# Performance work log

Measured on AMD Instinct MI355X. Metric: run time of the kernel, lower is better.

Reference implementation:

```python
import jax, jax.numpy as jnp
import numpy as np

B, H, S, D = 2, 16, 2048, 64


def _apply_rope(feats, cos, sin):
    # feats: [B,H,S,D]; cos,sin: [B,S,D//2] -> broadcast over heads
    c = cos[:, None, :, :]
    s = sin[:, None, :, :]
    x1, x2 = jnp.split(feats, 2, axis=-1)
    r1 = x1 * c - x2 * s
    r2 = x1 * s + x2 * c
    return jnp.concatenate([r1, r2], axis=-1)


def setup_inputs() -> dict:
    key = jax.random.key(0)
    kq, kk, kv, ka = jax.random.split(key, 4)
    q = jax.random.normal(kq, (B, H, S, D), dtype=jnp.float32)
    k = jax.random.normal(kk, (B, H, S, D), dtype=jnp.float32)
    v = jax.random.normal(kv, (B, H, S, D), dtype=jnp.float32)
    # geometry-derived rope angles -> cos/sin coefficients
    angles = jax.random.uniform(ka, (B, S, D // 2), dtype=jnp.float32,
                                minval=-np.pi, maxval=np.pi)
    return {"q": q, "k": k, "v": v,
            "cos": jnp.cos(angles), "sin": jnp.sin(angles)}


def reference(q, k, v, cos, sin):
    # Ray-conditioned RoPE on Q and K, then scaled dot-product attention.
    qr = _apply_rope(q, cos, sin)
    kr = _apply_rope(k, cos, sin)
    scale = 1.0 / jnp.sqrt(jnp.asarray(q.shape[-1], q.dtype))
    scores = jnp.einsum('bhqd,bhkd->bhqk', qr, kr) * scale  # [B,H,S,S]
    attn = jax.nn.softmax(scores, axis=-1)
    return jnp.einsum('bhqk,bhkd->bhqd', attn, v)
```

## Files before the change

kernel.cpp:

```cpp
#include <hip/hip_runtime.h>

#define NB 2
#define NH 16
#define SEQ 2048
#define DIM 64
#define SD (SEQ * DIM)

typedef short s16x8 __attribute__((ext_vector_type(8)));
typedef float f32x4 __attribute__((ext_vector_type(4)));
typedef float f32x16 __attribute__((ext_vector_type(16)));
typedef unsigned u32x4 __attribute__((ext_vector_type(4)));

typedef const __attribute__((address_space(1))) void* gas_t;
typedef __attribute__((address_space(3))) void* las_t;

__device__ __forceinline__ short f2bf(float f) {
  unsigned u = __float_as_uint(f);
  u += 0x7FFFu + ((u >> 16) & 1u);
  return (short)(u >> 16);
}

__device__ __forceinline__ float fast_exp2(float x) {
#if __has_builtin(__builtin_amdgcn_exp2f)
  return __builtin_amdgcn_exp2f(x);
#else
  float r;
  asm("v_exp_f32 %0, %1" : "=v"(r) : "v"(x));
  return r;
#endif
}

__global__ __launch_bounds__(256)
void prep_all(const float* __restrict__ q, const float* __restrict__ k,
              const float* __restrict__ v, const float* __restrict__ cg,
              const float* __restrict__ sg, short* __restrict__ qr,
              short* __restrict__ kr, short* __restrict__ vt) {
  const int tid = threadIdx.x;
  if (blockIdx.x < 1024) {
    const float QS = 0.125f * 1.44269504088896340736f;
    const int gt = blockIdx.x * 256 + tid;
    const int row = gt >> 2;
    const int dd = (gt & 3) * 8;
    const int s = row & (SEQ - 1);
    const int b = row >> 15;

    const float* qp = q + (size_t)row * DIM;
    const float* kp = k + (size_t)row * DIM;
    const float* cp = cg + ((size_t)b * SEQ + s) * (DIM / 2) + dd;
    const float* sp = sg + ((size_t)b * SEQ + s) * (DIM / 2) + dd;

    float q1[8], q2[8], k1[8], k2[8], cc[8], ss[8];
    *(f32x4*)&q1[0] = *(const f32x4*)(qp + dd);
    *(f32x4*)&q1[4] = *(const f32x4*)(qp + dd + 4);
    *(f32x4*)&q2[0] = *(const f32x4*)(qp + dd + 32);
    *(f32x4*)&q2[4] = *(const f32x4*)(qp + dd + 36);
    *(f32x4*)&k1[0] = *(const f32x4*)(kp + dd);
    *(f32x4*)&k1[4] = *(const f32x4*)(kp + dd + 4);
    *(f32x4*)&k2[0] = *(const f32x4*)(kp + dd + 32);
    *(f32x4*)&k2[4] = *(const f32x4*)(kp + dd + 36);
    *(f32x4*)&cc[0] = *(const f32x4*)(cp);
    *(f32x4*)&cc[4] = *(const f32x4*)(cp + 4);
    *(f32x4*)&ss[0] = *(const f32x4*)(sp);
    *(f32x4*)&ss[4] = *(const f32x4*)(sp + 4);

    s16x8 qo1, qo2, ko1, ko2;
#pragma unroll
    for (int j = 0; j < 8; ++j) {
      qo1[j] = f2bf((q1[j] * cc[j] - q2[j] * ss[j]) * QS);
      qo2[j] = f2bf((q1[j] * ss[j] + q2[j] * cc[j]) * QS);
      ko1[j] = f2bf(k1[j] * cc[j] - k2[j] * ss[j]);
      ko2[j] = f2bf(k1[j] * ss[j] + k2[j] * cc[j]);
    }
    *(s16x8*)&qr[(size_t)row * DIM + dd] = qo1;
    *(s16x8*)&qr[(size_t)row * DIM + dd + 32] = qo2;
    *(s16x8*)&kr[(size_t)row * DIM + dd] = ko1;
    *(s16x8*)&kr[(size_t)row * DIM + dd + 32] = ko2;
  } else {
    const int blk = blockIdx.x - 1024;
    const int bh = blk >> 5;
    const int tile = blk & 31;
    const int d = tid & 63;
    const int kg = tid >> 6;
    const float* vp = v + ((size_t)bh * SEQ + tile * 64 + kg * 16) * DIM + d;
    short* op = vt + (size_t)bh * SD + (size_t)(tile * 2 + (kg >> 1)) * (64 * 32)
                + d * 32 + (kg & 1) * 16;
    s16x8 w0, w1;
#pragma unroll
    for (int j = 0; j < 8; ++j) w0[j] = f2bf(vp[(size_t)j * DIM]);
#pragma unroll
    for (int j = 0; j < 8; ++j) w1[j] = f2bf(vp[(size_t)(j + 8) * DIM]);
    *(s16x8*)&op[0] = w0;
    *(s16x8*)&op[8] = w1;
  }
}

__global__ __launch_bounds__(256, 4)
void attn_main(const short* __restrict__ qr, const short* __restrict__ kr,
               const short* __restrict__ vt, float* __restrict__ out) {
  __shared__ __align__(16) short Kb[2][2][32 * 64];
  __shared__ __align__(16) short Vb[2][2][64 * 32];
  __shared__ float lred[2][32];

  const int nq = SEQ / 64;
  const int bid = blockIdx.x;
  const int cpx = gridDim.x >> 3;
  const int swz = (bid & 7) * cpx + (bid >> 3);
  const int bh = swz / nq;
  const int qb = swz % nq;

  const int tid = threadIdx.x;
  const int w = tid >> 6;
  const int kh = w >> 1;
  const int qs = w & 1;
  const int lane = tid & 63;
  const int n = lane & 31;
  const int h = lane >> 5;

  const int qw = qb * 64 + qs * 32;

  const short* qrp = qr + (size_t)bh * SD + (size_t)(qw + n) * DIM + 8 * h;
  s16x8 qa[4];
#pragma unroll
  for (int ds = 0; ds < 4; ++ds) qa[ds] = *(const s16x8*)(qrp + 16 * ds);

  int koff[2], voff[2];
#pragma unroll
  for (int i = 0; i < 2; ++i) {
    const int p = qs * 128 + i * 64 + lane;
    const int krow = p >> 3, kslot = p & 7;
    koff[i] = krow * 128 + ((kslot ^ (krow & 7)) * 16);
    const int vrow = p >> 2, vslot = p & 3;
    voff[i] = vrow * 64 + ((vslot ^ ((vrow >> 1) & 3)) * 16);
  }
  const char* kbh = (const char*)(kr + (size_t)bh * SD);
  const char* vbh = (const char*)(vt + (size_t)bh * SD);
  const int tbase = kh * 32;

  f32x16 Oa[2];
  Oa[0] = {};
  Oa[1] = {};
  float lp = 0.f;

#define STAGE(buf, t)                                                               \
  do {                                                                              \
    const char* ks_ = kbh + (size_t)(t) * 4096;                                     \
    const char* vs_ = vbh + (size_t)(t) * 4096;                                     \
    __builtin_amdgcn_global_load_lds((gas_t)(ks_ + koff[0]),                        \
                                     (las_t)&Kb[kh][buf][qs * 1024], 16, 0, 0);     \
    __builtin_amdgcn_global_load_lds((gas_t)(ks_ + koff[1]),                        \
                                     (las_t)&Kb[kh][buf][qs * 1024 + 512], 16, 0, 0); \
    __builtin_amdgcn_global_load_lds((gas_t)(vs_ + voff[0]),                        \
                                     (las_t)&Vb[kh][buf][qs * 1024], 16, 0, 0);     \
    __builtin_amdgcn_global_load_lds((gas_t)(vs_ + voff[1]),                        \
                                     (las_t)&Vb[kh][buf][qs * 1024 + 512], 16, 0, 0); \
  } while (0)

  STAGE(0, tbase);
  __syncthreads();
  int cur = 0;

#pragma unroll 2
  for (int it = 0; it < 32; ++it) {
    if (it < 31) STAGE(cur ^ 1, tbase + it + 1);

    s16x8 kf[4], vf[2][2];
#pragma unroll
    for (int ds = 0; ds < 4; ++ds)
      kf[ds] = *(const s16x8*)&Kb[kh][cur][n * 64 + (((2 * ds + h) ^ (n & 7)) * 8)];
#pragma unroll
    for (int dsub = 0; dsub < 2; ++dsub)
#pragma unroll
      for (int ks = 0; ks < 2; ++ks)
        vf[dsub][ks] = *(const s16x8*)&Vb[kh][cur][(dsub * 32 + n) * 32 +
                                                   (((2 * ks + h) ^ ((n >> 1) & 3)) * 8)];

    f32x16 S = {};
#pragma unroll
    for (int ds = 0; ds < 4; ++ds)
      S = __builtin_amdgcn_mfma_f32_32x32x16_bf16(kf[ds], qa[ds], S, 0, 0, 0);

    float e[16];
#pragma unroll
    for (int r = 0; r < 16; ++r) e[r] = fast_exp2(S[r]);
    {
      float s0 = (e[0] + e[1]) + (e[2] + e[3]);
      float s1 = (e[4] + e[5]) + (e[6] + e[7]);
      float s2 = (e[8] + e[9]) + (e[10] + e[11]);
      float s3 = (e[12] + e[13]) + (e[14] + e[15]);
      lp += (s0 + s1) + (s2 + s3);
    }

    unsigned pk[8];
#pragma unroll
    for (int i = 0; i < 8; ++i)
      asm("v_cvt_pk_bf16_f32 %0, %1, %2" : "=v"(pk[i]) : "v"(e[2 * i]), "v"(e[2 * i + 1]));
    s16x8 pa[2];
#pragma unroll
    for (int ksl = 0; ksl < 2; ++ksl) {
      unsigned a0 = pk[4 * ksl + 0], b0 = pk[4 * ksl + 2];
      unsigned a1 = pk[4 * ksl + 1], b1 = pk[4 * ksl + 3];
      asm("v_permlane32_swap_b32 %0, %1" : "+v"(a0), "+v"(b0));
      asm("v_permlane32_swap_b32 %0, %1" : "+v"(a1), "+v"(b1));
      u32x4 t;
      t[0] = a0; t[1] = a1; t[2] = b0; t[3] = b1;
      pa[ksl] = *(s16x8*)&t;
    }

#pragma unroll
    for (int dsub = 0; dsub < 2; ++dsub)
#pragma unroll
      for (int ksl = 0; ksl < 2; ++ksl)
        Oa[dsub] = __builtin_amdgcn_mfma_f32_32x32x16_bf16(pa[ksl], vf[dsub][ksl],
                                                           Oa[dsub], 0, 0, 0);

    __syncthreads();
    cur ^= 1;
  }
#undef STAGE

  lp += __shfl_xor(lp, 32);

  float* xch = (float*)&Kb[0][0][0];
  if (kh == 1) {
    float* ob = xch + qs * 2048;
#pragma unroll
    for (int r = 0; r < 16; ++r) {
      const int m = (r & 3) + 8 * (r >> 2) + 4 * h;
      ob[m * 64 + n] = Oa[0][r];
      ob[m * 64 + 32 + n] = Oa[1][r];
    }
    if (h == 0) lred[qs][n] = lp;
  }
  __syncthreads();
  if (kh == 0) {
    const float* pb = xch + qs * 2048;
    lp += lred[qs][n];
    const float invq = 1.0f / lp;
    float* og = out + ((size_t)bh * SEQ + qw) * DIM + n;
#pragma unroll
    for (int r = 0; r < 16; ++r) {
      const int m = (r & 3) + 8 * (r >> 2) + 4 * h;
      const float iv = __shfl(invq, m);
      og[(size_t)m * DIM] = (Oa[0][r] + pb[m * 64 + n]) * iv;
      og[(size_t)m * DIM + 32] = (Oa[1][r] + pb[m * 64 + 32 + n]) * iv;
    }
  }
}

__global__ __launch_bounds__(256, 2)
void rope_attn_mono(const float* __restrict__ qg, const float* __restrict__ kgl,
                    const float* __restrict__ vg, const float* __restrict__ cg,
                    const float* __restrict__ sg, float* __restrict__ out) {
  __shared__ __align__(16) short Kt[64 * DIM];
  __shared__ __align__(16) short Vt[DIM * 64];
  __shared__ __align__(16) short Pw[4][16 * 64];
  const int nq = SEQ / 64;
  const int bid = blockIdx.x;
  const int cpx = gridDim.x >> 3;
  const int swz = (bid & 7) * cpx + (bid >> 3);
  const int bh = swz / nq;
  const int qb = swz % nq;
  const int b = bh >> 4;
  const int tid = threadIdx.x;
  const int w = tid >> 6;
  const int lane = tid & 63;
  const int c = lane & 15;
  const int g = lane >> 4;
  const float* qbase = qg + (size_t)bh * SEQ * DIM;
  const float* kbase = kgl + (size_t)bh * SEQ * DIM;
  const float* vbase = vg + (size_t)bh * SEQ * DIM;
  const float* cbase = cg + (size_t)b * SEQ * (DIM / 2);
  const float* sbase = sg + (size_t)b * SEQ * (DIM / 2);
  const float QS = 0.125f * 1.44269504088896340736f;
  const int qrow = qb * 64 + w * 16 + c;
  const int d0 = g * 8;
  s16x8 qa0, qa1;
  {
    const float* qr = qbase + (size_t)qrow * DIM;
    const float* cr = cbase + (size_t)qrow * (DIM / 2);
    const float* sr = sbase + (size_t)qrow * (DIM / 2);
    float x1[8], x2[8], cc[8], ss[8];
    *(f32x4*)&x1[0] = *(const f32x4*)(qr + d0);
    *(f32x4*)&x1[4] = *(const f32x4*)(qr + d0 + 4);
    *(f32x4*)&x2[0] = *(const f32x4*)(qr + d0 + 32);
    *(f32x4*)&x2[4] = *(const f32x4*)(qr + d0 + 36);
    *(f32x4*)&cc[0] = *(const f32x4*)(cr + d0);
    *(f32x4*)&cc[4] = *(const f32x4*)(cr + d0 + 4);
    *(f32x4*)&ss[0] = *(const f32x4*)(sr + d0);
    *(f32x4*)&ss[4] = *(const f32x4*)(sr + d0 + 4);
#pragma unroll
    for (int j = 0; j < 8; ++j) {
      qa0[j] = f2bf((x1[j] * cc[j] - x2[j] * ss[j]) * QS);
      qa1[j] = f2bf((x1[j] * ss[j] + x2[j] * cc[j]) * QS);
    }
  }
  f32x4 Oa[4];
#pragma unroll
  for (int dt = 0; dt < 4; ++dt) { Oa[dt][0] = 0.f; Oa[dt][1] = 0.f; Oa[dt][2] = 0.f; Oa[dt][3] = 0.f; }
  float mrun[4], lrun[4];
#pragma unroll
  for (int r = 0; r < 4; ++r) { mrun[r] = -3.0e38f; lrun[r] = 0.f; }
  for (int kv = 0; kv < SEQ / 64; ++kv) {
    const int s0 = kv * 64;
#pragma unroll
    for (int rep = 0; rep < 2; ++rep) {
      const int id = tid + rep * 256;
      const int key = id >> 3;
      const int u = id & 7;
      const int srow = s0 + key;
      const float* krp = kbase + (size_t)srow * DIM;
      const float* cr = cbase + (size_t)srow * (DIM / 2);
      const float* sr = sbase + (size_t)srow * (DIM / 2);
      const int dd = (u & 3) * 8;
      float a[8], bb[8], cf[8], sf[8];
      *(f32x4*)&a[0] = *(const f32x4*)(krp + dd);
      *(f32x4*)&a[4] = *(const f32x4*)(krp + dd + 4);
      *(f32x4*)&bb[0] = *(const f32x4*)(krp + dd + 32);
      *(f32x4*)&bb[4] = *(const f32x4*)(krp + dd + 36);
      *(f32x4*)&cf[0] = *(const f32x4*)(cr + dd);
      *(f32x4*)&cf[4] = *(const f32x4*)(cr + dd + 4);
      *(f32x4*)&sf[0] = *(const f32x4*)(sr + dd);
      *(f32x4*)&sf[4] = *(const f32x4*)(sr + dd + 4);
      s16x8 wv;
      if (u < 4) {
#pragma unroll
        for (int j = 0; j < 8; ++j) wv[j] = f2bf(a[j] * cf[j] - bb[j] * sf[j]);
      } else {
#pragma unroll
        for (int j = 0; j < 8; ++j) wv[j] = f2bf(a[j] * sf[j] + bb[j] * cf[j]);
      }
      *(s16x8*)&Kt[key * DIM + ((u ^ (key & 7)) * 8)] = wv;
    }
    {
      const int d = tid & 63;
      const int kgp = tid >> 6;
      const float* vrow = vbase + (size_t)(s0 + kgp * 16) * DIM + d;
      s16x8 w0, w1;
#pragma unroll
      for (int j = 0; j < 8; ++j) w0[j] = f2bf(vrow[(size_t)j * DIM]);
#pragma unroll
      for (int j = 0; j < 8; ++j) w1[j] = f2bf(vrow[(size_t)(j + 8) * DIM]);
      *(s16x8*)&Vt[d * 64 + (((2 * kgp) ^ (d & 7)) * 8)] = w0;
      *(s16x8*)&Vt[d * 64 + (((2 * kgp + 1) ^ (d & 7)) * 8)] = w1;
    }
    __syncthreads();
    f32x4 sc[4];
#pragma unroll
    for (int kt = 0; kt < 4; ++kt) {
      const int key = kt * 16 + c;
      s16x8 b0 = *(const s16x8*)&Kt[key * DIM + ((g ^ (key & 7)) * 8)];
      s16x8 b1 = *(const s16x8*)&Kt[key * DIM + (((4 + g) ^ (key & 7)) * 8)];
      f32x4 z = {0.f, 0.f, 0.f, 0.f};
      z = __builtin_amdgcn_mfma_f32_16x16x32_bf16(qa0, b0, z, 0, 0, 0);
      z = __builtin_amdgcn_mfma_f32_16x16x32_bf16(qa1, b1, z, 0, 0, 0);
      sc[kt] = z;
    }
    float pf[4][4];
#pragma unroll
    for (int r = 0; r < 4; ++r) {
      float mt = fmaxf(fmaxf(sc[0][r], sc[1][r]), fmaxf(sc[2][r], sc[3][r]));
#pragma unroll
      for (int msk = 1; msk < 16; msk <<= 1) mt = fmaxf(mt, __shfl_xor(mt, msk));
      const float mnew = fmaxf(mrun[r], mt);
      const float corr = exp2f(mrun[r] - mnew);
      mrun[r] = mnew;
      float rs = 0.f;
#pragma unroll
      for (int kt = 0; kt < 4; ++kt) {
        const float p = exp2f(sc[kt][r] - mnew);
        pf[kt][r] = p;
        rs += p;
      }
#pragma unroll
      for (int msk = 1; msk < 16; msk <<= 1) rs += __shfl_xor(rs, msk);
      lrun[r] = lrun[r] * corr + rs;
#pragma unroll
      for (int dt = 0; dt < 4; ++dt) Oa[dt][r] *= corr;
    }
#pragma unroll
    for (int kt = 0; kt < 4; ++kt) {
      const int u = 2 * kt + (c >> 3);
      const int c7 = c & 7;
#pragma unroll
      for (int r = 0; r < 4; ++r) {
        const int qq = 4 * g + r;
        Pw[w][qq * 64 + ((u ^ (qq & 7)) * 8) + c7] = f2bf(pf[kt][r]);
      }
    }
    {
      const int qq = c;
      s16x8 pa0 = *(const s16x8*)&Pw[w][qq * 64 + ((g ^ (qq & 7)) * 8)];
      s16x8 pa1 = *(const s16x8*)&Pw[w][qq * 64 + (((4 + g) ^ (qq & 7)) * 8)];
#pragma unroll
      for (int dt = 0; dt < 4; ++dt) {
        const int d = dt * 16 + c;
        s16x8 v0 = *(const s16x8*)&Vt[d * 64 + ((g ^ (d & 7)) * 8)];
        s16x8 v1 = *(const s16x8*)&Vt[d * 64 + (((4 + g) ^ (d & 7)) * 8)];
        Oa[dt] = __builtin_amdgcn_mfma_f32_16x16x32_bf16(pa0, v0, Oa[dt], 0, 0, 0);
        Oa[dt] = __builtin_amdgcn_mfma_f32_16x16x32_bf16(pa1, v1, Oa[dt], 0, 0, 0);
      }
    }
    __syncthreads();
  }
  float* ob = out + ((size_t)bh * SEQ + (size_t)qb * 64 + (size_t)(w * 16)) * DIM;
#pragma unroll
  for (int r = 0; r < 4; ++r) {
    const float inv = 1.0f / lrun[r];
#pragma unroll
    for (int dt = 0; dt < 4; ++dt)
      ob[(size_t)(4 * g + r) * DIM + dt * 16 + c] = Oa[dt][r] * inv;
  }
}

extern "C" void kernel_launch(void* const* d_in, const int* in_sizes, int n_in,
                              void* d_out, int out_size, void* d_ws, size_t ws_size,
                              hipStream_t stream) {
  const float* q = (const float*)d_in[0];
  const float* k = (const float*)d_in[1];
  const float* v = (const float*)d_in[2];
  const float* cosv = (const float*)d_in[3];
  const float* sinv = (const float*)d_in[4];
  float* out = (float*)d_out;

  const size_t elems = (size_t)NB * NH * SEQ * DIM;
  const size_t need = 3 * elems * sizeof(short);

  if (ws_size >= need) {
    short* qrw = (short*)d_ws;
    short* krw = qrw + elems;
    short* vtw = krw + elems;
    hipLaunchKernelGGL(prep_all, dim3(2048), dim3(256), 0, stream,
                       q, k, v, cosv, sinv, qrw, krw, vtw);
    hipLaunchKernelGGL(attn_main, dim3(NB * NH * (SEQ / 64)), dim3(256), 0, stream,
                       qrw, krw, vtw, out);
  } else {
    hipLaunchKernelGGL(rope_attn_mono, dim3(NB * NH * (SEQ / 64)), dim3(256), 0, stream,
                       q, k, v, cosv, sinv, out);
  }
}
```

Baseline: 65.13 us.

## Split keys per wave with private LDS staging and no per-iteration barriers

Restructures attn_main so each of the four waves handles all 64 queries of the block over a private quarter of the key sequence. Each wave stages its own K/V tiles into a private double buffer and waits on them with s_waitcnt, which removes the block-wide __syncthreads per iteration and reuses each K/V fragment across two query sub-tiles. A four-way cross-wave reduction of outputs and row sums through LDS, with vectorized float4 stores, replaces the old two-way exchange. In exchange the kernel uses more registers (launch bounds lowered to 2 blocks per SIMD) and more LDS.

```diff
diff --git a/kernel.cpp b/kernel.cpp
--- a/kernel.cpp
+++ b/kernel.cpp
@@ -94,12 +94,11 @@
   }
 }
 
-__global__ __launch_bounds__(256, 4)
+__global__ __launch_bounds__(256, 2)
 void attn_main(const short* __restrict__ qr, const short* __restrict__ kr,
                const short* __restrict__ vt, float* __restrict__ out) {
-  __shared__ __align__(16) short Kb[2][2][32 * 64];
-  __shared__ __align__(16) short Vb[2][2][64 * 32];
-  __shared__ float lred[2][32];
+  __shared__ __align__(16) short St[4][2][4096];
+  __shared__ float lred[4][64];
 
   const int nq = SEQ / 64;
   const int bid = blockIdx.x;
@@ -110,23 +109,23 @@
 
   const int tid = threadIdx.x;
   const int w = tid >> 6;
-  const int kh = w >> 1;
-  const int qs = w & 1;
   const int lane = tid & 63;
   const int n = lane & 31;
   const int h = lane >> 5;
-
-  const int qw = qb * 64 + qs * 32;
-
-  const short* qrp = qr + (size_t)bh * SD + (size_t)(qw + n) * DIM + 8 * h;
-  s16x8 qa[4];
-#pragma unroll
-  for (int ds = 0; ds < 4; ++ds) qa[ds] = *(const s16x8*)(qrp + 16 * ds);
-
-  int koff[2], voff[2];
-#pragma unroll
-  for (int i = 0; i < 2; ++i) {
-    const int p = qs * 128 + i * 64 + lane;
+  const int qw = qb * 64;
+
+  s16x8 qa[2][4];
+#pragma unroll
+  for (int qs = 0; qs < 2; ++qs) {
+    const short* qrp = qr + (size_t)bh * SD + (size_t)(qw + qs * 32 + n) * DIM + 8 * h;
+#pragma unroll
+    for (int ds = 0; ds < 4; ++ds) qa[qs][ds] = *(const s16x8*)(qrp + 16 * ds);
+  }
+
+  int koff[4], voff[4];
+#pragma unroll
+  for (int i = 0; i < 4; ++i) {
+    const int p = i * 64 + lane;
     const int krow = p >> 3, kslot = p & 7;
     koff[i] = krow * 128 + ((kslot ^ (krow & 7)) * 16);
     const int vrow = p >> 2, vslot = p & 3;
@@ -134,115 +133,131 @@
   }
   const char* kbh = (const char*)(kr + (size_t)bh * SD);
   const char* vbh = (const char*)(vt + (size_t)bh * SD);
-  const int tbase = kh * 32;
-
-  f32x16 Oa[2];
-  Oa[0] = {};
-  Oa[1] = {};
-  float lp = 0.f;
-
-#define STAGE(buf, t)                                                               \
-  do {                                                                              \
-    const char* ks_ = kbh + (size_t)(t) * 4096;                                     \
-    const char* vs_ = vbh + (size_t)(t) * 4096;                                     \
-    __builtin_amdgcn_global_load_lds((gas_t)(ks_ + koff[0]),                        \
-                                     (las_t)&Kb[kh][buf][qs * 1024], 16, 0, 0);     \
-    __builtin_amdgcn_global_load_lds((gas_t)(ks_ + koff[1]),                        \
-                                     (las_t)&Kb[kh][buf][qs * 1024 + 512], 16, 0, 0); \
-    __builtin_amdgcn_global_load_lds((gas_t)(vs_ + voff[0]),                        \
-                                     (las_t)&Vb[kh][buf][qs * 1024], 16, 0, 0);     \
-    __builtin_amdgcn_global_load_lds((gas_t)(vs_ + voff[1]),                        \
-                                     (las_t)&Vb[kh][buf][qs * 1024 + 512], 16, 0, 0); \
+  const int tb = w * 16;
+
+  f32x16 Oa[2][2];
+  Oa[0][0] = {}; Oa[0][1] = {}; Oa[1][0] = {}; Oa[1][1] = {};
+  float lp[2] = {0.f, 0.f};
+
+#define STAGE(buf, t)                                                              \
+  do {                                                                             \
+    const char* ks_ = kbh + (size_t)(t) * 4096;                                    \
+    const char* vs_ = vbh + (size_t)(t) * 4096;                                    \
+    __builtin_amdgcn_global_load_lds((gas_t)(ks_ + koff[0]), (las_t)&St[w][buf][0], 16, 0, 0);    \
+    __builtin_amdgcn_global_load_lds((gas_t)(ks_ + koff[1]), (las_t)&St[w][buf][512], 16, 0, 0);  \
+    __builtin_amdgcn_global_load_lds((gas_t)(ks_ + koff[2]), (las_t)&St[w][buf][1024], 16, 0, 0); \
+    __builtin_amdgcn_global_load_lds((gas_t)(ks_ + koff[3]), (las_t)&St[w][buf][1536], 16, 0, 0); \
+    __builtin_amdgcn_global_load_lds((gas_t)(vs_ + voff[0]), (las_t)&St[w][buf][2048], 16, 0, 0); \
+    __builtin_amdgcn_global_load_lds((gas_t)(vs_ + voff[1]), (las_t)&St[w][buf][2560], 16, 0, 0); \
+    __builtin_amdgcn_global_load_lds((gas_t)(vs_ + voff[2]), (las_t)&St[w][buf][3072], 16, 0, 0); \
+    __builtin_amdgcn_global_load_lds((gas_t)(vs_ + voff[3]), (las_t)&St[w][buf][3584], 16, 0, 0); \
   } while (0)
 
-  STAGE(0, tbase);
+  STAGE(0, tb);
+  int cur = 0;
+
+  for (int it = 0; it < 16; ++it) {
+    asm volatile("s_waitcnt lgkmcnt(0)" ::: "memory");
+    if (it < 15) {
+      STAGE(cur ^ 1, tb + it + 1);
+      asm volatile("s_waitcnt vmcnt(8)" ::: "memory");
+    } else {
+      asm volatile("s_waitcnt vmcnt(0)" ::: "memory");
+    }
+    __builtin_amdgcn_sched_barrier(0);
+
+    const short* Kc = &St[w][cur][0];
+    const short* Vc = &St[w][cur][2048];
+    s16x8 kf[4], vf[2][2];
+#pragma unroll
+    for (int ds = 0; ds < 4; ++ds)
+      kf[ds] = *(const s16x8*)&Kc[n * 64 + (((2 * ds + h) ^ (n & 7)) * 8)];
+#pragma unroll
+    for (int dsub = 0; dsub < 2; ++dsub)
+#pragma unroll
+      for (int ks = 0; ks < 2; ++ks) {
+        const int vr = dsub * 32 + n;
+        vf[dsub][ks] = *(const s16x8*)&Vc[vr * 32 + (((2 * ks + h) ^ ((vr >> 1) & 3)) * 8)];
+      }
+
+#pragma unroll
+    for (int qs = 0; qs < 2; ++qs) {
+      f32x16 S = {};
+#pragma unroll
+      for (int ds = 0; ds < 4; ++ds)
+        S = __builtin_amdgcn_mfma_f32_32x32x16_bf16(kf[ds], qa[qs][ds], S, 0, 0, 0);
+
+      float e[16];
+#pragma unroll
+      for (int r = 0; r < 16; ++r) e[r] = fast_exp2(S[r]);
+      {
+        float s0 = (e[0] + e[1]) + (e[2] + e[3]);
+        float s1 = (e[4] + e[5]) + (e[6] + e[7]);
+        float s2 = (e[8] + e[9]) + (e[10] + e[11]);
+        float s3 = (e[12] + e[13]) + (e[14] + e[15]);
+        lp[qs] += (s0 + s1) + (s2 + s3);
+      }
+
+      unsigned pk[8];
+#pragma unroll
+      for (int i = 0; i < 8; ++i)
+        asm("v_cvt_pk_bf16_f32 %0, %1, %2" : "=v"(pk[i]) : "v"(e[2 * i]), "v"(e[2 * i + 1]));
+      s16x8 pa[2];
+#pragma unroll
+      for (int ksl = 0; ksl < 2; ++ksl) {
+        unsigned a0 = pk[4 * ksl + 0], b0 = pk[4 * ksl + 2];
+        unsigned a1 = pk[4 * ksl + 1], b1 = pk[4 * ksl + 3];
+        asm("v_permlane32_swap_b32 %0, %1" : "+v"(a0), "+v"(b0));
+        asm("v_permlane32_swap_b32 %0, %1" : "+v"(a1), "+v"(b1));
+        u32x4 t;
+        t[0] = a0; t[1] = a1; t[2] = b0; t[3] = b1;
+        pa[ksl] = *(s16x8*)&t;
+      }
+
+#pragma unroll
+      for (int dsub = 0; dsub < 2; ++dsub)
+#pragma unroll
+        for (int ksl = 0; ksl < 2; ++ksl)
+          Oa[qs][dsub] = __builtin_amdgcn_mfma_f32_32x32x16_bf16(pa[ksl], vf[dsub][ksl],
+                                                                 Oa[qs][dsub], 0, 0, 0);
+    }
+    cur ^= 1;
+  }
+#undef STAGE
+
+  {
+    float* ow = (float*)&St[w][0][0];
+#pragma unroll
+    for (int qs = 0; qs < 2; ++qs) {
+      lp[qs] += __shfl_xor(lp[qs], 32);
+#pragma unroll
+      for (int dsub = 0; dsub < 2; ++dsub)
+#pragma unroll
+        for (int r = 0; r < 16; ++r) {
+          const int q = qs * 32 + (r & 3) + 8 * (r >> 2) + 4 * h;
+          ow[q * 64 + dsub * 32 + n] = Oa[qs][dsub][r];
+        }
+      if (h == 0) lred[w][qs * 32 + n] = lp[qs];
+    }
+  }
   __syncthreads();
-  int cur = 0;
-
-#pragma unroll 2
-  for (int it = 0; it < 32; ++it) {
-    if (it < 31) STAGE(cur ^ 1, tbase + it + 1);
-
-    s16x8 kf[4], vf[2][2];
-#pragma unroll
-    for (int ds = 0; ds < 4; ++ds)
-      kf[ds] = *(const s16x8*)&Kb[kh][cur][n * 64 + (((2 * ds + h) ^ (n & 7)) * 8)];
-#pragma unroll
-    for (int dsub = 0; dsub < 2; ++dsub)
-#pragma unroll
-      for (int ks = 0; ks < 2; ++ks)
-        vf[dsub][ks] = *(const s16x8*)&Vb[kh][cur][(dsub * 32 + n) * 32 +
-                                                   (((2 * ks + h) ^ ((n >> 1) & 3)) * 8)];
-
-    f32x16 S = {};
-#pragma unroll
-    for (int ds = 0; ds < 4; ++ds)
-      S = __builtin_amdgcn_mfma_f32_32x32x16_bf16(kf[ds], qa[ds], S, 0, 0, 0);
-
-    float e[16];
-#pragma unroll
-    for (int r = 0; r < 16; ++r) e[r] = fast_exp2(S[r]);
-    {
-      float s0 = (e[0] + e[1]) + (e[2] + e[3]);
-      float s1 = (e[4] + e[5]) + (e[6] + e[7]);
-      float s2 = (e[8] + e[9]) + (e[10] + e[11]);
-      float s3 = (e[12] + e[13]) + (e[14] + e[15]);
-      lp += (s0 + s1) + (s2 + s3);
-    }
-
-    unsigned pk[8];
-#pragma unroll
-    for (int i = 0; i < 8; ++i)
-      asm("v_cvt_pk_bf16_f32 %0, %1, %2" : "=v"(pk[i]) : "v"(e[2 * i]), "v"(e[2 * i + 1]));
-    s16x8 pa[2];
-#pragma unroll
-    for (int ksl = 0; ksl < 2; ++ksl) {
-      unsigned a0 = pk[4 * ksl + 0], b0 = pk[4 * ksl + 2];
-      unsigned a1 = pk[4 * ksl + 1], b1 = pk[4 * ksl + 3];
-      asm("v_permlane32_swap_b32 %0, %1" : "+v"(a0), "+v"(b0));
-      asm("v_permlane32_swap_b32 %0, %1" : "+v"(a1), "+v"(b1));
-      u32x4 t;
-      t[0] = a0; t[1] = a1; t[2] = b0; t[3] = b1;
-      pa[ksl] = *(s16x8*)&t;
-    }
-
-#pragma unroll
-    for (int dsub = 0; dsub < 2; ++dsub)
-#pragma unroll
-      for (int ksl = 0; ksl < 2; ++ksl)
-        Oa[dsub] = __builtin_amdgcn_mfma_f32_32x32x16_bf16(pa[ksl], vf[dsub][ksl],
-                                                           Oa[dsub], 0, 0, 0);
-
-    __syncthreads();
-    cur ^= 1;
-  }
-#undef STAGE
-
-  lp += __shfl_xor(lp, 32);
-
-  float* xch = (float*)&Kb[0][0][0];
-  if (kh == 1) {
-    float* ob = xch + qs * 2048;
-#pragma unroll
-    for (int r = 0; r < 16; ++r) {
-      const int m = (r & 3) + 8 * (r >> 2) + 4 * h;
-      ob[m * 64 + n] = Oa[0][r];
-      ob[m * 64 + 32 + n] = Oa[1][r];
-    }
-    if (h == 0) lred[qs][n] = lp;
-  }
-  __syncthreads();
-  if (kh == 0) {
-    const float* pb = xch + qs * 2048;
-    lp += lred[qs][n];
-    const float invq = 1.0f / lp;
-    float* og = out + ((size_t)bh * SEQ + qw) * DIM + n;
-#pragma unroll
-    for (int r = 0; r < 16; ++r) {
-      const int m = (r & 3) + 8 * (r >> 2) + 4 * h;
-      const float iv = __shfl(invq, m);
-      og[(size_t)m * DIM] = (Oa[0][r] + pb[m * 64 + n]) * iv;
-      og[(size_t)m * DIM + 32] = (Oa[1][r] + pb[m * 64 + 32 + n]) * iv;
+  {
+    const float* xch = (const float*)&St[0][0][0];
+    const int rsub = lane >> 4;
+    const int dc = (lane & 15) * 4;
+    float* og = out + ((size_t)bh * SEQ + qw) * DIM;
+#pragma unroll
+    for (int rg = 0; rg < 4; ++rg) {
+      const int q = w * 16 + rg * 4 + rsub;
+      f32x4 a0 = *(const f32x4*)&xch[0 * 4096 + q * 64 + dc];
+      f32x4 a1 = *(const f32x4*)&xch[1 * 4096 + q * 64 + dc];
+      f32x4 a2 = *(const f32x4*)&xch[2 * 4096 + q * 64 + dc];
+      f32x4 a3 = *(const f32x4*)&xch[3 * 4096 + q * 64 + dc];
+      const float lt = (lred[0][q] + lred[1][q]) + (lred[2][q] + lred[3][q]);
+      const float iv = 1.0f / lt;
+      f32x4 r = (a0 + a1) + (a2 + a3);
+      r[0] *= iv; r[1] *= iv; r[2] *= iv; r[3] *= iv;
+      *(f32x4*)(og + (size_t)q * 64 + dc) = r;
     }
   }
 }
```

After: 62.75 us. -3.7%, faster.
